# Optimization experiments

Measured on AMD Instinct MI355X. Metric: run time of the kernel, lower is better.

Reference implementation:

```python
import jax, jax.numpy as jnp
import numpy as np

N_EMBD = 1024
N_HEADS = 16
HEAD_SIZE = N_EMBD // N_HEADS
B, T = 1, 4096
LN_EPS = 1e-5


def setup_inputs() -> dict:
    key = jax.random.key(0)
    ks = jax.random.split(key, 12)
    s = lambda fan_in: 1.0 / np.sqrt(fan_in)
    return {
        "x": jax.random.normal(ks[0], (B, T, N_EMBD), dtype=jnp.float32),
        # per-head Q/K/V projections (no bias), stacked over heads: [H, C, hd]
        "Wq": jax.random.normal(ks[1], (N_HEADS, N_EMBD, HEAD_SIZE), dtype=jnp.float32) * s(N_EMBD),
        "Wk": jax.random.normal(ks[2], (N_HEADS, N_EMBD, HEAD_SIZE), dtype=jnp.float32) * s(N_EMBD),
        "Wv": jax.random.normal(ks[3], (N_HEADS, N_EMBD, HEAD_SIZE), dtype=jnp.float32) * s(N_EMBD),
        # output projection (with bias)
        "Wp": jax.random.normal(ks[4], (N_EMBD, N_EMBD), dtype=jnp.float32) * s(N_EMBD),
        "bp": jnp.zeros((N_EMBD,), dtype=jnp.float32),
        # FFN: Linear(C, 4C) -> ReLU -> Linear(4C, C)
        "W1": jax.random.normal(ks[5], (N_EMBD, 4 * N_EMBD), dtype=jnp.float32) * s(N_EMBD),
        "b1": jnp.zeros((4 * N_EMBD,), dtype=jnp.float32),
        "W2": jax.random.normal(ks[6], (4 * N_EMBD, N_EMBD), dtype=jnp.float32) * s(4 * N_EMBD),
        "b2": jnp.zeros((N_EMBD,), dtype=jnp.float32),
        # LayerNorms
        "g1": jnp.ones((N_EMBD,), dtype=jnp.float32),
        "be1": jnp.zeros((N_EMBD,), dtype=jnp.float32),
        "g2": jnp.ones((N_EMBD,), dtype=jnp.float32),
        "be2": jnp.zeros((N_EMBD,), dtype=jnp.float32),
    }


def _layernorm(x, gamma, beta):
    mu = jnp.mean(x, axis=-1, keepdims=True)
    var = jnp.mean(jnp.square(x - mu), axis=-1, keepdims=True)
    return (x - mu) * jax.lax.rsqrt(var + LN_EPS) * gamma + beta


def _block(x, Wq, Wk, Wv, Wp, bp, W1, b1, W2, b2, g1, be1, g2, be2):
    Bn, Tn, C = x.shape
    h = _layernorm(x, g1, be1)
    # per-head projections: [B, H, T, hd]
    q = jnp.einsum("btc,hcd->bhtd", h, Wq)
    k = jnp.einsum("btc,hcd->bhtd", h, Wk)
    v = jnp.einsum("btc,hcd->bhtd", h, Wv)
    # NOTE: original scales by C**-0.5 where C = n_embd (not head_size)
    scores = jnp.einsum("bhtd,bhsd->bhts", q, k) * (C ** -0.5)
    causal = jnp.tril(jnp.ones((Tn, Tn), dtype=bool))
    scores = jnp.where(causal, scores, -jnp.inf)
    w = jax.nn.softmax(scores, axis=-1)
    attn = jnp.einsum("bhts,bhsd->bhtd", w, v)
    # concat heads: [B, T, H*hd] = [B, T, C]
    attn = attn.transpose(0, 2, 1, 3).reshape(Bn, Tn, C)
    x = x + attn @ Wp + bp
    h2 = _layernorm(x, g2, be2)
    ff = jax.nn.relu(h2 @ W1 + b1) @ W2 + b2
    return x + ff


def reference(x, Wq, Wk, Wv, Wp, bp, W1, b1, W2, b2, g1, be1, g2, be2):
    return _block(x, Wq, Wk, Wv, Wp, bp, W1, b1, W2, b2, g1, be1, g2, be2)
```

## Files before the change

### kernel.cpp

```cpp
#include <hip/hip_runtime.h>
#include <cstdint>

typedef __attribute__((ext_vector_type(8))) short bf16x8;
typedef __attribute__((ext_vector_type(4))) float f32x4;
typedef __attribute__((ext_vector_type(16))) float f32x16;
typedef __attribute__((ext_vector_type(4))) unsigned int u32x4;

__device__ __forceinline__ short f2b(float f) {
  unsigned u = __builtin_bit_cast(unsigned, f);
  unsigned r = (u + 0x7fffu + ((u >> 16) & 1u)) >> 16;
  return (short)(unsigned short)r;
}
__device__ __forceinline__ float b2f(short s) {
  unsigned u = ((unsigned)(unsigned short)s) << 16;
  return __builtin_bit_cast(float, u);
}

__device__ __forceinline__ void gload16(void* lds_dst, const void* gsrc) {
  __builtin_amdgcn_global_load_lds(
      (const __attribute__((address_space(1))) void*)gsrc,
      (__attribute__((address_space(3))) void*)lds_dst, 16, 0, 0);
}

__device__ __forceinline__ unsigned cvtpk(float a, float b) {
// ... 115 lines not shown
}

__global__ void vtrans(const short* __restrict__ qkv, short* __restrict__ Vt)
{
  __shared__ short tl[32][33];
  const int t0 = blockIdx.x * 32;
  const int c0 = blockIdx.y * 32;
  const int head = c0 >> 6, d0 = c0 & 63;
  const int tx = threadIdx.x;
#pragma unroll
  for (int i2 = 0; i2 < 4; ++i2) {
    int i = threadIdx.y + i2 * 8;
    tl[i][tx] = qkv[(long)(t0 + i) * 3072 + 2048 + c0 + tx];
  }
  __syncthreads();
#pragma unroll
  for (int i2 = 0; i2 < 4; ++i2) {
    int i = threadIdx.y + i2 * 8;
    Vt[(long)head * 262144 + (long)(d0 + i) * 4096 + t0 + tx] = tl[tx][i];
  }
}

__global__ __launch_bounds__(256)
void layernorm_bf16(const float* __restrict__ x, const float* __restrict__ g,
                    const float* __restrict__ be, short* __restrict__ outp)
{
  const int row = blockIdx.x;
  const int t = threadIdx.x;
  const float4 v = ((const float4*)(x + (long)row * 1024))[t];
  float s = v.x + v.y + v.z + v.w;
  float ss = v.x * v.x + v.y * v.y + v.z * v.z + v.w * v.w;
#pragma unroll
  for (int off = 1; off < 64; off <<= 1) {
    s += __shfl_xor(s, off);
    ss += __shfl_xor(ss, off);
  }
  __shared__ float red[8];
  const int wave = t >> 6, lane = t & 63;
  if (lane == 0) { red[wave] = s; red[4 + wave] = ss; }
  __syncthreads();
  s = red[0] + red[1] + red[2] + red[3];
  ss = red[4] + red[5] + red[6] + red[7];
  const float mu = s * (1.f / 1024.f);
  const float rstd = rsqrtf(ss * (1.f / 1024.f) - mu * mu + 1e-5f);
  const float4 gv = ((const float4*)g)[t];
  const float4 bv = ((const float4*)be)[t];
  short4 ov;
  ov.x = f2b((v.x - mu) * rstd * gv.x + bv.x);
  ov.y = f2b((v.y - mu) * rstd * gv.y + bv.y);
  ov.z = f2b((v.z - mu) * rstd * gv.z + bv.z);
  ov.w = f2b((v.w - mu) * rstd * gv.w + bv.w);
  *(short4*)(outp + (long)row * 1024 + t * 4) = ov;
}

template<int EPI>
__global__ __launch_bounds__(512, 2)
void gemm128(const short* __restrict__ A, const short* __restrict__ Bt,
             int N, int K, int NT,
             short* __restrict__ Cb, float* __restrict__ Cf,
             const float* __restrict__ bias, const float* __restrict__ resid)
{
  __shared__ __align__(16) short As[2 * 8192];
  __shared__ __align__(16) short Bs[2 * 8192];
  const int tid = threadIdx.x;
  const int lane = tid & 63;
  const int wave = tid >> 6;
  const int wm = wave >> 2;
  const int wn = wave & 3;
  const int l15 = lane & 15, lg = lane >> 4;

  const int nwg = gridDim.x * gridDim.y;
  const int lin = blockIdx.y * gridDim.x + blockIdx.x;
  const int swz = (lin & 7) * (nwg >> 3) + (lin >> 3);
  const long m0 = (long)(swz / gridDim.x) * 128;
  const long n0 = (long)(swz % gridDim.x) * 128;

  const int rloc = lane >> 3;
  const int csrc = (lane & 7) ^ rloc;
  const short* Ag = A + (m0 + wave * 8 + rloc) * K + csrc * 8;
  const short* Bg = Bt + (n0 + wave * 8 + rloc) * K + csrc * 8;
  const int wbase = wave * 512;

  f32x4 acc[4][2] = {};

#define STAGE128(buf, kt)                                                     \
  do {                                                                        \
    gload16(As + (buf) * 8192 + wbase, Ag + (kt));                            \
    gload16(As + (buf) * 8192 + 4096 + wbase, Ag + (long)64 * K + (kt));      \
    gload16(Bs + (buf) * 8192 + wbase, Bg + (kt));                            \
    gload16(Bs + (buf) * 8192 + 4096 + wbase, Bg + (long)64 * K + (kt));      \
  } while (0)

  STAGE128(0, 0);
  STAGE128(1, 64);
  asm volatile("s_waitcnt vmcnt(4)" ::: "memory");
  __builtin_amdgcn_sched_barrier(0);
  __builtin_amdgcn_s_barrier();
  __builtin_amdgcn_sched_barrier(0);

  const int cA = l15 & 7;
  for (int t = 0; t < NT; ++t) {
    const char* Ab = (const char*)(As + (t & 1) * 8192);
    const char* Bb = (const char*)(Bs + (t & 1) * 8192);
#pragma unroll
    for (int kk = 0; kk < 2; ++kk) {
      bf16x8 af[4], bk[2];
#pragma unroll
      for (int mi = 0; mi < 4; ++mi)
        af[mi] = *(const bf16x8*)(Ab + (wm * 64 + mi * 16 + l15) * 128 + 16 * ((kk * 4 + lg) ^ cA));
#pragma unroll
      for (int ni = 0; ni < 2; ++ni)
        bk[ni] = *(const bf16x8*)(Bb + (wn * 32 + ni * 16 + l15) * 128 + 16 * ((kk * 4 + lg) ^ cA));
      __builtin_amdgcn_s_setprio(1);
#pragma unroll
      for (int mi = 0; mi < 4; ++mi)
#pragma unroll
        for (int ni = 0; ni < 2; ++ni)
          acc[mi][ni] = __builtin_amdgcn_mfma_f32_16x16x32_bf16(af[mi], bk[ni], acc[mi][ni], 0, 0, 0);
      __builtin_amdgcn_s_setprio(0);
    }
    if (t == NT - 1) break;
    __builtin_amdgcn_s_barrier();
    __builtin_amdgcn_sched_barrier(0);
    if (t + 2 < NT) {
      STAGE128(t & 1, (long)(t + 2) * 64);
      asm volatile("s_waitcnt vmcnt(4)" ::: "memory");
    } else {
      asm volatile("s_waitcnt vmcnt(0)" ::: "memory");
    }
    __builtin_amdgcn_sched_barrier(0);
    __builtin_amdgcn_s_barrier();
    __builtin_amdgcn_sched_barrier(0);
  }
#undef STAGE128

#pragma unroll
  for (int mi = 0; mi < 4; ++mi) {
#pragma unroll
    for (int ni = 0; ni < 2; ++ni) {
      const long col = n0 + wn * 32 + ni * 16 + l15;
#pragma unroll
      for (int r = 0; r < 4; ++r) {
        const long row = m0 + wm * 64 + mi * 16 + lg * 4 + r;
        const long idx = row * N + col;
        float v = acc[mi][ni][r];
        if (EPI == 0) {
          Cb[idx] = f2b(v);
        } else {
          Cf[idx] = v + bias[col] + resid[idx];
        }
      }
    }
  }
}

__device__ __forceinline__ void stage256(short* AsB, short* BsB,
                                         const short* Ag, const short* Bg,
                                         long kt, int K, int ldsoff)
{
#pragma unroll
  for (int p = 0; p < 4; ++p)
    gload16(AsB + p * 4096 + ldsoff, Ag + (long)p * 64 * K + kt);
#pragma unroll
  for (int p = 0; p < 4; ++p)
    gload16(BsB + p * 4096 + ldsoff, Bg + (long)p * 64 * K + kt);
}

template<int EPI>
__global__ __launch_bounds__(512, 2)
void gemm256(const short* __restrict__ A, const short* __restrict__ Bt,
             int N, int K, int NT,
             short* __restrict__ Cb, const float* __restrict__ bias)
{
  __shared__ __align__(16) short As[2 * 16384];
  __shared__ __align__(16) short Bs[2 * 16384];
  const int tid = threadIdx.x;
  const int lane = tid & 63;
  const int wave = tid >> 6;
  const int wm = wave >> 2;
  const int wn = wave & 3;
  const int l15 = lane & 15, lg = lane >> 4;

  const int nwg = gridDim.x * gridDim.y;
  const int lin = blockIdx.y * gridDim.x + blockIdx.x;
  const int swz = (lin & 7) * (nwg >> 3) + (lin >> 3);
  const long m0 = (long)(swz / gridDim.x) * 256;
  const long n0 = (long)(swz % gridDim.x) * 256;

  const int trow = tid >> 3;
  const int csrc = (tid & 7) ^ (trow & 7);
  const short* Ag = A + (m0 + trow) * K + csrc * 8;
  const short* Bg = Bt + (n0 + trow) * K + csrc * 8;
  const int ldsoff = wave * 512;

  f32x4 acc[8][4] = {};

  stage256(As, Bs, Ag, Bg, 0, K, ldsoff);
  asm volatile("s_waitcnt vmcnt(0)" ::: "memory");
  __builtin_amdgcn_sched_barrier(0);
  __builtin_amdgcn_s_barrier();
  __builtin_amdgcn_sched_barrier(0);

  const int cA = l15 & 7;
  for (int t = 0; t < NT; ++t) {
    const char* Ab = (const char*)(As + (t & 1) * 16384);
    const char* Bb = (const char*)(Bs + (t & 1) * 16384);
    short* Asn = As + ((t + 1) & 1) * 16384;
    short* Bsn = Bs + ((t + 1) & 1) * 16384;
    const bool more = (t + 1 < NT);
    const long ktn = (long)(t + 1) * 64;
    bf16x8 bk[4];
#pragma unroll
    for (int ph = 0; ph < 4; ++ph) {
      const int kk = ph >> 1;
      const int mh = (ph & 1) * 4;
      bf16x8 af[4];
#pragma unroll
      for (int mi = 0; mi < 4; ++mi)
        af[mi] = *(const bf16x8*)(Ab + (wm * 128 + (mh + mi) * 16 + l15) * 128 + 16 * ((kk * 4 + lg) ^ cA));
      if ((ph & 1) == 0) {
#pragma unroll
        for (int ni = 0; ni < 4; ++ni)
          bk[ni] = *(const bf16x8*)(Bb + (wn * 64 + ni * 16 + l15) * 128 + 16 * ((kk * 4 + lg) ^ cA));
      }
      if (more && ph == 0) {
#pragma unroll
        for (int p = 0; p < 4; ++p)
          gload16(Asn + p * 4096 + ldsoff, Ag + (long)p * 64 * K + ktn);
      }
      if (more && ph == 1) {
#pragma unroll
        for (int p = 0; p < 4; ++p)
          gload16(Bsn + p * 4096 + ldsoff, Bg + (long)p * 64 * K + ktn);
      }
      __builtin_amdgcn_s_barrier();
      asm volatile("s_waitcnt lgkmcnt(0)" ::: "memory");
      __builtin_amdgcn_sched_barrier(0);
      __builtin_amdgcn_s_setprio(1);
#pragma unroll
      for (int mi = 0; mi < 4; ++mi)
#pragma unroll
        for (int ni = 0; ni < 4; ++ni)
          acc[mh + mi][ni] = __builtin_amdgcn_mfma_f32_16x16x32_bf16(af[mi], bk[ni], acc[mh + mi][ni], 0, 0, 0);
      __builtin_amdgcn_s_setprio(0);
      if (ph == 3 && more) {
        asm volatile("s_waitcnt vmcnt(0)" ::: "memory");
        __builtin_amdgcn_sched_barrier(0);
      }
      __builtin_amdgcn_s_barrier();
      __builtin_amdgcn_sched_barrier(0);
    }
  }

#pragma unroll
  for (int mi = 0; mi < 8; ++mi) {
#pragma unroll
    for (int ni = 0; ni < 4; ++ni) {
      const long col = n0 + wn * 64 + ni * 16 + l15;
      const float bb = (EPI == 2) ? bias[col] : 0.f;
#pragma unroll
      for (int r = 0; r < 4; ++r) {
        const long row = m0 + wm * 128 + mi * 16 + lg * 4 + r;
        float v = acc[mi][ni][r];
        if (EPI == 2) { v += bb; v = v > 0.f ? v : 0.f; }
        Cb[row * N + col] = f2b(v);
      }
    }
  }
}

__device__ __forceinline__ void stage_k32(short* lds, const short* gRowBase)
{
  const int lane = threadIdx.x & 63;
  const int rloc = lane >> 3;
  const int cs = (lane & 7) ^ rloc;
#pragma unroll
  for (int p = 0; p < 4; ++p)
    gload16(lds + p * 512, gRowBase + (long)(p * 8 + rloc) * 3072 + cs * 8);
}
__device__ __forceinline__ void stage_v32(short* lds, const short* vHeadBase, int t0)
{
  const int lane = threadIdx.x & 63;
  const int rloc = lane >> 3;
  const int cs = (lane & 7) ^ rloc;
#pragma unroll
  for (int p = 0; p < 4; ++p) {
    const int row = p * 8 + rloc;
    const int d = row + ((cs & 4) << 3);
    gload16(lds + p * 512, vHeadBase + (long)d * 4096 + t0 + (cs & 3) * 8);
  }
}

__global__ __launch_bounds__(256)
void attn_fwd6(const short* __restrict__ qkv, const short* __restrict__ Vt,
               short* __restrict__ outp)
{
  __shared__ __align__(16) short POOL[4 * 4096];
  __shared__ float lAll[64];
  short* const OB = POOL;

  const int tid = threadIdx.x;
  const int lane = tid & 63;
  const int wave = tid >> 6;
  const int wq = wave & 1;
  const int ks = wave >> 1;
  const int l31 = lane & 31;
  const int h = lane >> 5;
  const int rs = l31 & 7;

  const int id = blockIdx.x;
  const int head = ((id & 7) << 1) | (id >> 8);
  const int bx = (id >> 3) & 31;

  const short* Qg = qkv + head * 64;
  const short* Kg = qkv + 1024 + head * 64;
  const short* Vg = Vt + (long)head * 262144;

  short* Kw = POOL + wave * 4096;

  bf16x8 onesf;
#pragma unroll
  for (int j = 0; j < 8; ++j) onesf[j] = (short)0x3F80;

  for (int ph = 0; ph < 2; ++ph) {
    const int qsuper = ph ? (63 - bx) : bx;
    const int q0 = qsuper * 64 + wq * 32;
    const int q = q0 + l31;
    const int nt = qsuper + 1;

    bf16x8 qf[4];
#pragma unroll
    for (int d = 0; d < 4; ++d) {
      bf16x8 tq = *(const bf16x8*)(Qg + (long)q * 3072 + d * 16 + h * 8);
#pragma unroll
      for (int j = 0; j < 8; ++j) tq[j] = f2b(b2f(tq[j]) * (0.03125f * 1.44269504f));
      qf[d] = tq;
    }

    f32x16 o0 = {}, o1 = {}, lacc = {};

    stage_k32(Kw, Kg + (long)(ks * 32) * 3072);
    stage_v32(Kw + 2048, Vg, ks * 32);

    for (int t = 0; t < nt; ++t) {
      asm volatile("s_waitcnt vmcnt(0)" ::: "memory");
      __builtin_amdgcn_sched_barrier(0);
      const char* Kb = (const char*)Kw;
      const char* Vb = Kb + 4096;
      const bf16x8 kf0 = *(const bf16x8*)(Kb + l31 * 128 + 16 * ((0 + h) ^ rs));
      const bf16x8 kf1 = *(const bf16x8*)(Kb + l31 * 128 + 16 * ((2 + h) ^ rs));
      const bf16x8 kf2 = *(const bf16x8*)(Kb + l31 * 128 + 16 * ((4 + h) ^ rs));
      const bf16x8 kf3 = *(const bf16x8*)(Kb + l31 * 128 + 16 * ((6 + h) ^ rs));
      const bf16x8 vf00 = *(const bf16x8*)(Vb + l31 * 128 + 16 * ((0 + h) ^ rs));
      const bf16x8 vf01 = *(const bf16x8*)(Vb + l31 * 128 + 16 * ((2 + h) ^ rs));
      const bf16x8 vf10 = *(const bf16x8*)(Vb + l31 * 128 + 16 * ((4 + h) ^ rs));
      const bf16x8 vf11 = *(const bf16x8*)(Vb + l31 * 128 + 16 * ((6 + h) ^ rs));
      asm volatile("s_waitcnt lgkmcnt(0)" ::: "memory");
      __builtin_amdgcn_sched_barrier(0);
      if (t + 1 < nt) {
        stage_k32(Kw, Kg + (long)((t + 1) * 64 + ks * 32) * 3072);
        stage_v32(Kw + 2048, Vg, (t + 1) * 64 + ks * 32);
      }
      f32x16 s = {};
      __builtin_amdgcn_s_setprio(1);
      s = __builtin_amdgcn_mfma_f32_32x32x16_bf16(kf0, qf[0], s, 0, 0, 0);
      s = __builtin_amdgcn_mfma_f32_32x32x16_bf16(kf1, qf[1], s, 0, 0, 0);
      s = __builtin_amdgcn_mfma_f32_32x32x16_bf16(kf2, qf[2], s, 0, 0, 0);
      s = __builtin_amdgcn_mfma_f32_32x32x16_bf16(kf3, qf[3], s, 0, 0, 0);
      __builtin_amdgcn_s_setprio(0);
      if (t == qsuper) {
        const int kb0 = t * 64 + ks * 32 + 4 * h;
#pragma unroll
        for (int r = 0; r < 16; ++r) {
          const int k0 = kb0 + (r & 3) + 8 * (r >> 2);
          if (k0 > q) s[r] = -INFINITY;
        }
      }
#pragma unroll
      for (int r = 0; r < 16; ++r) s[r] = exp2x(s[r]);
      unsigned P0 = cvtpk(s[0], s[1]),   P1 = cvtpk(s[2], s[3]);
      unsigned P2 = cvtpk(s[4], s[5]),   P3 = cvtpk(s[6], s[7]);
      unsigned P4 = cvtpk(s[8], s[9]),   P5 = cvtpk(s[10], s[11]);
      unsigned P6 = cvtpk(s[12], s[13]), P7 = cvtpk(s[14], s[15]);
      plswap(P0, P2); plswap(P1, P3); plswap(P4, P6); plswap(P5, P7);
      u32x4 f0, f1;
      f0[0] = P0; f0[1] = P1; f0[2] = P2; f0[3] = P3;
      f1[0] = P4; f1[1] = P5; f1[2] = P6; f1[3] = P7;
      const bf16x8 pa0 = __builtin_bit_cast(bf16x8, f0);
      const bf16x8 pa1 = __builtin_bit_cast(bf16x8, f1);
      __builtin_amdgcn_s_setprio(1);
      o0 = __builtin_amdgcn_mfma_f32_32x32x16_bf16(pa0, vf00, o0, 0, 0, 0);
      o0 = __builtin_amdgcn_mfma_f32_32x32x16_bf16(pa1, vf01, o0, 0, 0, 0);
      o1 = __builtin_amdgcn_mfma_f32_32x32x16_bf16(pa0, vf10, o1, 0, 0, 0);
      o1 = __builtin_amdgcn_mfma_f32_32x32x16_bf16(pa1, vf11, o1, 0, 0, 0);
      lacc = __builtin_amdgcn_mfma_f32_32x32x16_bf16(pa0, onesf, lacc, 0, 0, 0);
      lacc = __builtin_amdgcn_mfma_f32_32x32x16_bf16(pa1, onesf, lacc, 0, 0, 0);
      __builtin_amdgcn_s_setprio(0);
    }

    __syncthreads();
    if (ks == 1) {
#pragma unroll
      for (int r = 0; r < 16; ++r) {
        const int qq = wq * 32 + (r & 3) + 8 * (r >> 2) + 4 * h;
        OB[qq * 64 + l31] = f2b(o0[r]);
        OB[qq * 64 + 32 + l31] = f2b(o1[r]);
      }
      if (l31 == 0) {
#pragma unroll
        for (int r = 0; r < 16; ++r) {
          const int qq = wq * 32 + (r & 3) + 8 * (r >> 2) + 4 * h;
          lAll[qq] = lacc[r];
        }
      }
    }
    __syncthreads();
    if (ks == 0) {
#pragma unroll
      for (int r = 0; r < 16; ++r) {
        const int qq = wq * 32 + (r & 3) + 8 * (r >> 2) + 4 * h;
        const float inv = 1.f / (lacc[r] + lAll[qq]);
        const long qr = (long)qsuper * 64 + qq;
        const float v0 = o0[r] + b2f(OB[qq * 64 + l31]);
        const float v1 = o1[r] + b2f(OB[qq * 64 + 32 + l31]);
        outp[qr * 1024 + head * 64 + l31] = f2b(v0 * inv);
        outp[qr * 1024 + head * 64 + 32 + l31] = f2b(v1 * inv);
      }
    }
    __syncthreads();
  }
}

extern "C" void kernel_launch(void* const* d_in, const int* in_sizes, int n_in,
                              void* d_out, int out_size, void* d_ws, size_t ws_size,
                              hipStream_t stream)
{
  (void)in_sizes; (void)n_in; (void)out_size; (void)ws_size;
  const float* x   = (const float*)d_in[0];
  const float* Wq  = (const float*)d_in[1];
  const float* Wk  = (const float*)d_in[2];
  const float* Wv  = (const float*)d_in[3];
  const float* Wp  = (const float*)d_in[4];
  const float* bp  = (const float*)d_in[5];
  const float* W1  = (const float*)d_in[6];
  const float* b1  = (const float*)d_in[7];
  const float* W2  = (const float*)d_in[8];
  const float* b2  = (const float*)d_in[9];
  const float* g1  = (const float*)d_in[10];
  const float* be1 = (const float*)d_in[11];
  const float* g2  = (const float*)d_in[12];
  const float* be2 = (const float*)d_in[13];
  float* out = (float*)d_out;

  char* ws = (char*)d_ws;
  const size_t MB = 1ull << 20;
  short* WqkvT = (short*)(ws + 0 * MB);
  short* WpT   = (short*)(ws + 6 * MB);
  short* W1T   = (short*)(ws + 8 * MB);
  short* W2T   = (short*)(ws + 16 * MB);
  short* hbuf  = (short*)(ws + 24 * MB);
  short* qkvb  = (short*)(ws + 32 * MB);
  short* attnb = (short*)(ws + 56 * MB);
  float* x1    = (float*)(ws + 64 * MB);
  short* Vtb   = (short*)(ws + 64 * MB);

  prep_all<<<16384, 256, 0, stream>>>(Wq, Wk, Wv, Wp, W1, W2, x, g1, be1,
                                      WqkvT, WpT, W1T, W2T, hbuf);
  gemm256<0><<<dim3(12, 16), 512, 0, stream>>>(hbuf, WqkvT, 3072, 1024, 16,
                                               qkvb, nullptr);
  vtrans<<<dim3(128, 32), dim3(32, 8), 0, stream>>>(qkvb, Vtb);
  attn_fwd6<<<512, 256, 0, stream>>>(qkvb, Vtb, attnb);
  gemm128<1><<<dim3(8, 32), 512, 0, stream>>>(attnb, WpT, 1024, 1024, 16,
                                              nullptr, x1, bp, x);
  layernorm_bf16<<<4096, 256, 0, stream>>>(x1, g2, be2, hbuf);
  gemm256<2><<<dim3(16, 16), 512, 0, stream>>>(hbuf, W1T, 4096, 1024, 16,
                                               qkvb, b1);
  gemm128<1><<<dim3(8, 32), 512, 0, stream>>>(qkvb, W2T, 1024, 4096, 64,
                                              nullptr, out, b2, x1);
}
```

Measured before the change: 246.8 us.

## Split attention KV range by tile parity and merge partials in a separate kernel

```diff
diff --git a/kernel.cpp b/kernel.cpp
--- a/kernel.cpp
+++ b/kernel.cpp
@@ -431,8 +431,9 @@
 }
 
 __global__ __launch_bounds__(256)
-void attn_fwd6(const short* __restrict__ qkv, const short* __restrict__ Vt,
-               short* __restrict__ outp)
+void attn_fwd7(const short* __restrict__ qkv, const short* __restrict__ Vt,
+               short* __restrict__ P0buf, short* __restrict__ P1buf,
+               float* __restrict__ lbuf)
 {
   __shared__ __align__(16) short POOL[4 * 4096];
   __shared__ float lAll[64];
@@ -448,12 +449,17 @@
   const int rs = l31 & 7;
 
   const int id = blockIdx.x;
-  const int head = ((id & 7) << 1) | (id >> 8);
-  const int bx = (id >> 3) & 31;
+  const int xcd = id & 7;
+  const int k = id >> 3;
+  const int head = (xcd << 1) | (k & 1);
+  const int qp = k >> 1;
+  const int qsuper = 63 - (qp >> 1);
+  const int parity = qp & 1;
 
   const short* Qg = qkv + head * 64;
   const short* Kg = qkv + 1024 + head * 64;
   const short* Vg = Vt + (long)head * 262144;
+  short* Pout = parity ? P1buf : P0buf;
 
   short* Kw = POOL + wave * 4096;
 
@@ -461,113 +467,133 @@
 #pragma unroll
   for (int j = 0; j < 8; ++j) onesf[j] = (short)0x3F80;
 
-  for (int ph = 0; ph < 2; ++ph) {
-    const int qsuper = ph ? (63 - bx) : bx;
-    const int q0 = qsuper * 64 + wq * 32;
-    const int q = q0 + l31;
-    const int nt = qsuper + 1;
-
-    bf16x8 qf[4];
-#pragma unroll
-    for (int d = 0; d < 4; ++d) {
-      bf16x8 tq = *(const bf16x8*)(Qg + (long)q * 3072 + d * 16 + h * 8);
-#pragma unroll
-      for (int j = 0; j < 8; ++j) tq[j] = f2b(b2f(tq[j]) * (0.03125f * 1.44269504f));
-      qf[d] = tq;
-    }
-
-    f32x16 o0 = {}, o1 = {}, lacc = {};
-
-    stage_k32(Kw, Kg + (long)(ks * 32) * 3072);
-    stage_v32(Kw + 2048, Vg, ks * 32);
-
-    for (int t = 0; t < nt; ++t) {
-      asm volatile("s_waitcnt vmcnt(0)" ::: "memory");
-      __builtin_amdgcn_sched_barrier(0);
-      const char* Kb = (const char*)Kw;
-      const char* Vb = Kb + 4096;
-      const bf16x8 kf0 = *(const bf16x8*)(Kb + l31 * 128 + 16 * ((0 + h) ^ rs));
-      const bf16x8 kf1 = *(const bf16x8*)(Kb + l31 * 128 + 16 * ((2 + h) ^ rs));
-      const bf16x8 kf2 = *(const bf16x8*)(Kb + l31 * 128 + 16 * ((4 + h) ^ rs));
-      const bf16x8 kf3 = *(const bf16x8*)(Kb + l31 * 128 + 16 * ((6 + h) ^ rs));
-      const bf16x8 vf00 = *(const bf16x8*)(Vb + l31 * 128 + 16 * ((0 + h) ^ rs));
-      const bf16x8 vf01 = *(const bf16x8*)(Vb + l31 * 128 + 16 * ((2 + h) ^ rs));
-      const bf16x8 vf10 = *(const bf16x8*)(Vb + l31 * 128 + 16 * ((4 + h) ^ rs));
-      const bf16x8 vf11 = *(const bf16x8*)(Vb + l31 * 128 + 16 * ((6 + h) ^ rs));
-      asm volatile("s_waitcnt lgkmcnt(0)" ::: "memory");
-      __builtin_amdgcn_sched_barrier(0);
-      if (t + 1 < nt) {
-        stage_k32(Kw, Kg + (long)((t + 1) * 64 + ks * 32) * 3072);
-        stage_v32(Kw + 2048, Vg, (t + 1) * 64 + ks * 32);
-      }
-      f32x16 s = {};
-      __builtin_amdgcn_s_setprio(1);
-      s = __builtin_amdgcn_mfma_f32_32x32x16_bf16(kf0, qf[0], s, 0, 0, 0);
-      s = __builtin_amdgcn_mfma_f32_32x32x16_bf16(kf1, qf[1], s, 0, 0, 0);
-      s = __builtin_amdgcn_mfma_f32_32x32x16_bf16(kf2, qf[2], s, 0, 0, 0);
-      s = __builtin_amdgcn_mfma_f32_32x32x16_bf16(kf3, qf[3], s, 0, 0, 0);
-      __builtin_amdgcn_s_setprio(0);
-      if (t == qsuper) {
-        const int kb0 = t * 64 + ks * 32 + 4 * h;
-#pragma unroll
-        for (int r = 0; r < 16; ++r) {
-          const int k0 = kb0 + (r & 3) + 8 * (r >> 2);
-          if (k0 > q) s[r] = -INFINITY;
-        }
-      }
-#pragma unroll
-      for (int r = 0; r < 16; ++r) s[r] = exp2x(s[r]);
-      unsigned P0 = cvtpk(s[0], s[1]),   P1 = cvtpk(s[2], s[3]);
-      unsigned P2 = cvtpk(s[4], s[5]),   P3 = cvtpk(s[6], s[7]);
-      unsigned P4 = cvtpk(s[8], s[9]),   P5 = cvtpk(s[10], s[11]);
-      unsigned P6 = cvtpk(s[12], s[13]), P7 = cvtpk(s[14], s[15]);
-      plswap(P0, P2); plswap(P1, P3); plswap(P4, P6); plswap(P5, P7);
-      u32x4 f0, f1;
-      f0[0] = P0; f0[1] = P1; f0[2] = P2; f0[3] = P3;
-      f1[0] = P4; f1[1] = P5; f1[2] = P6; f1[3] = P7;
-      const bf16x8 pa0 = __builtin_bit_cast(bf16x8, f0);
-      const bf16x8 pa1 = __builtin_bit_cast(bf16x8, f1);
-      __builtin_amdgcn_s_setprio(1);
-      o0 = __builtin_amdgcn_mfma_f32_32x32x16_bf16(pa0, vf00, o0, 0, 0, 0);
-      o0 = __builtin_amdgcn_mfma_f32_32x32x16_bf16(pa1, vf01, o0, 0, 0, 0);
-      o1 = __builtin_amdgcn_mfma_f32_32x32x16_bf16(pa0, vf10, o1, 0, 0, 0);
-      o1 = __builtin_amdgcn_mfma_f32_32x32x16_bf16(pa1, vf11, o1, 0, 0, 0);
-      lacc = __builtin_amdgcn_mfma_f32_32x32x16_bf16(pa0, onesf, lacc, 0, 0, 0);
-      lacc = __builtin_amdgcn_mfma_f32_32x32x16_bf16(pa1, onesf, lacc, 0, 0, 0);
-      __builtin_amdgcn_s_setprio(0);
-    }
-
-    __syncthreads();
-    if (ks == 1) {
+  const int q0 = qsuper * 64 + wq * 32;
+  const int q = q0 + l31;
+  const int nt = qsuper + 1;
+
+  bf16x8 qf[4];
+#pragma unroll
+  for (int d = 0; d < 4; ++d) {
+    bf16x8 tq = *(const bf16x8*)(Qg + (long)q * 3072 + d * 16 + h * 8);
+#pragma unroll
+    for (int j = 0; j < 8; ++j) tq[j] = f2b(b2f(tq[j]) * (0.03125f * 1.44269504f));
+    qf[d] = tq;
+  }
+
+  f32x16 o0 = {}, o1 = {}, lacc = {};
+
+  if (parity < nt) {
+    stage_k32(Kw, Kg + (long)(parity * 64 + ks * 32) * 3072);
+    stage_v32(Kw + 2048, Vg, parity * 64 + ks * 32);
+  }
+
+  for (int t = parity; t < nt; t += 2) {
+    asm volatile("s_waitcnt vmcnt(0)" ::: "memory");
+    __builtin_amdgcn_sched_barrier(0);
+    const char* Kb = (const char*)Kw;
+    const char* Vb = Kb + 4096;
+    const bf16x8 kf0 = *(const bf16x8*)(Kb + l31 * 128 + 16 * ((0 + h) ^ rs));
+    const bf16x8 kf1 = *(const bf16x8*)(Kb + l31 * 128 + 16 * ((2 + h) ^ rs));
+    const bf16x8 kf2 = *(const bf16x8*)(Kb + l31 * 128 + 16 * ((4 + h) ^ rs));
+    const bf16x8 kf3 = *(const bf16x8*)(Kb + l31 * 128 + 16 * ((6 + h) ^ rs));
+    const bf16x8 vf00 = *(const bf16x8*)(Vb + l31 * 128 + 16 * ((0 + h) ^ rs));
+    const bf16x8 vf01 = *(const bf16x8*)(Vb + l31 * 128 + 16 * ((2 + h) ^ rs));
+    const bf16x8 vf10 = *(const bf16x8*)(Vb + l31 * 128 + 16 * ((4 + h) ^ rs));
+    const bf16x8 vf11 = *(const bf16x8*)(Vb + l31 * 128 + 16 * ((6 + h) ^ rs));
+    asm volatile("s_waitcnt lgkmcnt(0)" ::: "memory");
+    __builtin_amdgcn_sched_barrier(0);
+    if (t + 2 < nt) {
+      stage_k32(Kw, Kg + (long)((t + 2) * 64 + ks * 32) * 3072);
+      stage_v32(Kw + 2048, Vg, (t + 2) * 64 + ks * 32);
+    }
+    f32x16 s = {};
+    __builtin_amdgcn_s_setprio(1);
+    s = __builtin_amdgcn_mfma_f32_32x32x16_bf16(kf0, qf[0], s, 0, 0, 0);
+    s = __builtin_amdgcn_mfma_f32_32x32x16_bf16(kf1, qf[1], s, 0, 0, 0);
+    s = __builtin_amdgcn_mfma_f32_32x32x16_bf16(kf2, qf[2], s, 0, 0, 0);
+    s = __builtin_amdgcn_mfma_f32_32x32x16_bf16(kf3, qf[3], s, 0, 0, 0);
+    __builtin_amdgcn_s_setprio(0);
+    if (t == qsuper) {
+      const int kb0 = t * 64 + ks * 32 + 4 * h;
+#pragma unroll
+      for (int r = 0; r < 16; ++r) {
+        const int k0 = kb0 + (r & 3) + 8 * (r >> 2);
+        if (k0 > q) s[r] = -INFINITY;
+      }
+    }
+#pragma unroll
+    for (int r = 0; r < 16; ++r) s[r] = exp2x(s[r]);
+    unsigned P0 = cvtpk(s[0], s[1]),   P1 = cvtpk(s[2], s[3]);
+    unsigned P2 = cvtpk(s[4], s[5]),   P3 = cvtpk(s[6], s[7]);
+    unsigned P4 = cvtpk(s[8], s[9]),   P5 = cvtpk(s[10], s[11]);
+    unsigned P6 = cvtpk(s[12], s[13]), P7 = cvtpk(s[14], s[15]);
+    plswap(P0, P2); plswap(P1, P3); plswap(P4, P6); plswap(P5, P7);
+    u32x4 f0, f1;
+    f0[0] = P0; f0[1] = P1; f0[2] = P2; f0[3] = P3;
+    f1[0] = P4; f1[1] = P5; f1[2] = P6; f1[3] = P7;
+    const bf16x8 pa0 = __builtin_bit_cast(bf16x8, f0);
+    const bf16x8 pa1 = __builtin_bit_cast(bf16x8, f1);
+    __builtin_amdgcn_s_setprio(1);
+    o0 = __builtin_amdgcn_mfma_f32_32x32x16_bf16(pa0, vf00, o0, 0, 0, 0);
+    o0 = __builtin_amdgcn_mfma_f32_32x32x16_bf16(pa1, vf01, o0, 0, 0, 0);
+    o1 = __builtin_amdgcn_mfma_f32_32x32x16_bf16(pa0, vf10, o1, 0, 0, 0);
+    o1 = __builtin_amdgcn_mfma_f32_32x32x16_bf16(pa1, vf11, o1, 0, 0, 0);
+    lacc = __builtin_amdgcn_mfma_f32_32x32x16_bf16(pa0, onesf, lacc, 0, 0, 0);
+    lacc = __builtin_amdgcn_mfma_f32_32x32x16_bf16(pa1, onesf, lacc, 0, 0, 0);
+    __builtin_amdgcn_s_setprio(0);
+  }
+
+  __syncthreads();
+  if (ks == 1) {
+#pragma unroll
+    for (int r = 0; r < 16; ++r) {
+      const int qq = wq * 32 + (r & 3) + 8 * (r >> 2) + 4 * h;
+      OB[qq * 64 + l31] = f2b(o0[r]);
+      OB[qq * 64 + 32 + l31] = f2b(o1[r]);
+    }
+    if (l31 == 0) {
 #pragma unroll
       for (int r = 0; r < 16; ++r) {
         const int qq = wq * 32 + (r & 3) + 8 * (r >> 2) + 4 * h;
-        OB[qq * 64 + l31] = f2b(o0[r]);
-        OB[qq * 64 + 32 + l31] = f2b(o1[r]);
-      }
-      if (l31 == 0) {
-#pragma unroll
-        for (int r = 0; r < 16; ++r) {
-          const int qq = wq * 32 + (r & 3) + 8 * (r >> 2) + 4 * h;
-          lAll[qq] = lacc[r];
-        }
-      }
-    }
-    __syncthreads();
-    if (ks == 0) {
-#pragma unroll
-      for (int r = 0; r < 16; ++r) {
-        const int qq = wq * 32 + (r & 3) + 8 * (r >> 2) + 4 * h;
-        const float inv = 1.f / (lacc[r] + lAll[qq]);
-        const long qr = (long)qsuper * 64 + qq;
-        const float v0 = o0[r] + b2f(OB[qq * 64 + l31]);
-        const float v1 = o1[r] + b2f(OB[qq * 64 + 32 + l31]);
-        outp[qr * 1024 + head * 64 + l31] = f2b(v0 * inv);
-        outp[qr * 1024 + head * 64 + 32 + l31] = f2b(v1 * inv);
-      }
-    }
-    __syncthreads();
-  }
+        lAll[qq] = lacc[r];
+      }
+    }
+  }
+  __syncthreads();
+  if (ks == 0) {
+#pragma unroll
+    for (int r = 0; r < 16; ++r) {
+      const int qq = wq * 32 + (r & 3) + 8 * (r >> 2) + 4 * h;
+      const long qr = (long)qsuper * 64 + qq;
+      const float v0 = o0[r] + b2f(OB[qq * 64 + l31]);
+      const float v1 = o1[r] + b2f(OB[qq * 64 + 32 + l31]);
+      Pout[qr * 1024 + head * 64 + l31] = f2b(v0);
+      Pout[qr * 1024 + head * 64 + 32 + l31] = f2b(v1);
+      if (l31 == 0)
+        lbuf[(long)parity * 65536 + head * 4096 + qr] = lacc[r] + lAll[qq];
+    }
+  }
+}
+
+__global__ __launch_bounds__(256)
+void merge_attn(const short* __restrict__ P0, const short* __restrict__ P1,
+                const float* __restrict__ lbuf, short* __restrict__ outp)
+{
+  const int q = blockIdx.x;
+  const int t = threadIdx.x;
+  const int head = t >> 4;
+  const float l0 = lbuf[head * 4096 + q];
+  const float l1 = lbuf[65536 + head * 4096 + q];
+  const float inv = 1.f / (l0 + l1);
+  const long base = (long)q * 1024 + t * 4;
+  short4 a = *(const short4*)(P0 + base);
+  short4 b = *(const short4*)(P1 + base);
+  short4 o;
+  o.x = f2b((b2f(a.x) + b2f(b.x)) * inv);
+  o.y = f2b((b2f(a.y) + b2f(b.y)) * inv);
+  o.z = f2b((b2f(a.z) + b2f(b.z)) * inv);
+  o.w = f2b((b2f(a.w) + b2f(b.w)) * inv);
+  *(short4*)(outp + base) = o;
 }
 
 extern "C" void kernel_launch(void* const* d_in, const int* in_sizes, int n_in,
@@ -602,13 +628,16 @@
   short* attnb = (short*)(ws + 56 * MB);
   float* x1    = (float*)(ws + 64 * MB);
   short* Vtb   = (short*)(ws + 64 * MB);
+  float* lbuf  = (float*)(ws + 0 * MB);
+  short* P1buf = hbuf;
 
   prep_all<<<16384, 256, 0, stream>>>(Wq, Wk, Wv, Wp, W1, W2, x, g1, be1,
                                       WqkvT, WpT, W1T, W2T, hbuf);
   gemm256<0><<<dim3(12, 16), 512, 0, stream>>>(hbuf, WqkvT, 3072, 1024, 16,
                                                qkvb, nullptr);
   vtrans<<<dim3(128, 32), dim3(32, 8), 0, stream>>>(qkvb, Vtb);
-  attn_fwd6<<<512, 256, 0, stream>>>(qkvb, Vtb, attnb);
+  attn_fwd7<<<2048, 256, 0, stream>>>(qkvb, Vtb, attnb, P1buf, lbuf);
+  merge_attn<<<4096, 256, 0, stream>>>(attnb, P1buf, lbuf, attnb);
   gemm128<1><<<dim3(8, 32), 512, 0, stream>>>(attnb, WpT, 1024, 1024, 16,
                                               nullptr, x1, bp, x);
   layernorm_bf16<<<4096, 256, 0, stream>>>(x1, g2, be2, hbuf);
```

Result: slower. 254.8 us (+3.2%).

## Process both paired query tiles in one K/V sweep in attention

Applied to the files above, without the earlier changes.

```diff
diff --git a/kernel.cpp b/kernel.cpp
--- a/kernel.cpp
+++ b/kernel.cpp
@@ -431,7 +431,7 @@
 }
 
 __global__ __launch_bounds__(256)
-void attn_fwd6(const short* __restrict__ qkv, const short* __restrict__ Vt,
+void attn_fwd8(const short* __restrict__ qkv, const short* __restrict__ Vt,
                short* __restrict__ outp)
 {
   __shared__ __align__(16) short POOL[4 * 4096];
@@ -450,6 +450,7 @@
   const int id = blockIdx.x;
   const int head = ((id & 7) << 1) | (id >> 8);
   const int bx = (id >> 3) & 31;
+  const int qsA = bx, qsB = 63 - bx;
 
   const short* Qg = qkv + head * 64;
   const short* Kg = qkv + 1024 + head * 64;
@@ -461,66 +462,78 @@
 #pragma unroll
   for (int j = 0; j < 8; ++j) onesf[j] = (short)0x3F80;
 
-  for (int ph = 0; ph < 2; ++ph) {
-    const int qsuper = ph ? (63 - bx) : bx;
-    const int q0 = qsuper * 64 + wq * 32;
-    const int q = q0 + l31;
-    const int nt = qsuper + 1;
-
-    bf16x8 qf[4];
-#pragma unroll
-    for (int d = 0; d < 4; ++d) {
-      bf16x8 tq = *(const bf16x8*)(Qg + (long)q * 3072 + d * 16 + h * 8);
-#pragma unroll
-      for (int j = 0; j < 8; ++j) tq[j] = f2b(b2f(tq[j]) * (0.03125f * 1.44269504f));
-      qf[d] = tq;
-    }
-
-    f32x16 o0 = {}, o1 = {}, lacc = {};
-
-    stage_k32(Kw, Kg + (long)(ks * 32) * 3072);
-    stage_v32(Kw + 2048, Vg, ks * 32);
-
-    for (int t = 0; t < nt; ++t) {
-      asm volatile("s_waitcnt vmcnt(0)" ::: "memory");
-      __builtin_amdgcn_sched_barrier(0);
-      const char* Kb = (const char*)Kw;
-      const char* Vb = Kb + 4096;
-      const bf16x8 kf0 = *(const bf16x8*)(Kb + l31 * 128 + 16 * ((0 + h) ^ rs));
-      const bf16x8 kf1 = *(const bf16x8*)(Kb + l31 * 128 + 16 * ((2 + h) ^ rs));
-      const bf16x8 kf2 = *(const bf16x8*)(Kb + l31 * 128 + 16 * ((4 + h) ^ rs));
-      const bf16x8 kf3 = *(const bf16x8*)(Kb + l31 * 128 + 16 * ((6 + h) ^ rs));
-      const bf16x8 vf00 = *(const bf16x8*)(Vb + l31 * 128 + 16 * ((0 + h) ^ rs));
-      const bf16x8 vf01 = *(const bf16x8*)(Vb + l31 * 128 + 16 * ((2 + h) ^ rs));
-      const bf16x8 vf10 = *(const bf16x8*)(Vb + l31 * 128 + 16 * ((4 + h) ^ rs));
-      const bf16x8 vf11 = *(const bf16x8*)(Vb + l31 * 128 + 16 * ((6 + h) ^ rs));
-      asm volatile("s_waitcnt lgkmcnt(0)" ::: "memory");
-      __builtin_amdgcn_sched_barrier(0);
-      if (t + 1 < nt) {
-        stage_k32(Kw, Kg + (long)((t + 1) * 64 + ks * 32) * 3072);
-        stage_v32(Kw + 2048, Vg, (t + 1) * 64 + ks * 32);
-      }
-      f32x16 s = {};
-      __builtin_amdgcn_s_setprio(1);
-      s = __builtin_amdgcn_mfma_f32_32x32x16_bf16(kf0, qf[0], s, 0, 0, 0);
-      s = __builtin_amdgcn_mfma_f32_32x32x16_bf16(kf1, qf[1], s, 0, 0, 0);
-      s = __builtin_amdgcn_mfma_f32_32x32x16_bf16(kf2, qf[2], s, 0, 0, 0);
-      s = __builtin_amdgcn_mfma_f32_32x32x16_bf16(kf3, qf[3], s, 0, 0, 0);
-      __builtin_amdgcn_s_setprio(0);
-      if (t == qsuper) {
-        const int kb0 = t * 64 + ks * 32 + 4 * h;
-#pragma unroll
-        for (int r = 0; r < 16; ++r) {
-          const int k0 = kb0 + (r & 3) + 8 * (r >> 2);
-          if (k0 > q) s[r] = -INFINITY;
-        }
-      }
-#pragma unroll
-      for (int r = 0; r < 16; ++r) s[r] = exp2x(s[r]);
-      unsigned P0 = cvtpk(s[0], s[1]),   P1 = cvtpk(s[2], s[3]);
-      unsigned P2 = cvtpk(s[4], s[5]),   P3 = cvtpk(s[6], s[7]);
-      unsigned P4 = cvtpk(s[8], s[9]),   P5 = cvtpk(s[10], s[11]);
-      unsigned P6 = cvtpk(s[12], s[13]), P7 = cvtpk(s[14], s[15]);
+  const int q0A = qsA * 64 + wq * 32, qA = q0A + l31;
+  const int q0B = qsB * 64 + wq * 32, qB = q0B + l31;
+  const int nt = qsB + 1;
+
+  bf16x8 qfA[4], qfB[4];
+#pragma unroll
+  for (int d = 0; d < 4; ++d) {
+    bf16x8 ta = *(const bf16x8*)(Qg + (long)qA * 3072 + d * 16 + h * 8);
+    bf16x8 tb = *(const bf16x8*)(Qg + (long)qB * 3072 + d * 16 + h * 8);
+#pragma unroll
+    for (int j = 0; j < 8; ++j) {
+      ta[j] = f2b(b2f(ta[j]) * (0.03125f * 1.44269504f));
+      tb[j] = f2b(b2f(tb[j]) * (0.03125f * 1.44269504f));
+    }
+    qfA[d] = ta;
+    qfB[d] = tb;
+  }
+
+  f32x16 oA0 = {}, oA1 = {}, lA = {};
+  f32x16 oB0 = {}, oB1 = {}, lB = {};
+
+  stage_k32(Kw, Kg + (long)(ks * 32) * 3072);
+  stage_v32(Kw + 2048, Vg, ks * 32);
+
+  for (int t = 0; t < nt; ++t) {
+    asm volatile("s_waitcnt vmcnt(0)" ::: "memory");
+    __builtin_amdgcn_sched_barrier(0);
+    const char* Kb = (const char*)Kw;
+    const char* Vb = Kb + 4096;
+    const bf16x8 kf0 = *(const bf16x8*)(Kb + l31 * 128 + 16 * ((0 + h) ^ rs));
+    const bf16x8 kf1 = *(const bf16x8*)(Kb + l31 * 128 + 16 * ((2 + h) ^ rs));
+    const bf16x8 kf2 = *(const bf16x8*)(Kb + l31 * 128 + 16 * ((4 + h) ^ rs));
+    const bf16x8 kf3 = *(const bf16x8*)(Kb + l31 * 128 + 16 * ((6 + h) ^ rs));
+    const bf16x8 vf00 = *(const bf16x8*)(Vb + l31 * 128 + 16 * ((0 + h) ^ rs));
+    const bf16x8 vf01 = *(const bf16x8*)(Vb + l31 * 128 + 16 * ((2 + h) ^ rs));
+    const bf16x8 vf10 = *(const bf16x8*)(Vb + l31 * 128 + 16 * ((4 + h) ^ rs));
+    const bf16x8 vf11 = *(const bf16x8*)(Vb + l31 * 128 + 16 * ((6 + h) ^ rs));
+    asm volatile("s_waitcnt lgkmcnt(0)" ::: "memory");
+    __builtin_amdgcn_sched_barrier(0);
+    if (t + 1 < nt) {
+      stage_k32(Kw, Kg + (long)((t + 1) * 64 + ks * 32) * 3072);
+      stage_v32(Kw + 2048, Vg, (t + 1) * 64 + ks * 32);
+    }
+    const bool doA = (t <= qsA);
+    f32x16 sB = {}, sA = {};
+    __builtin_amdgcn_s_setprio(1);
+    sB = __builtin_amdgcn_mfma_f32_32x32x16_bf16(kf0, qfB[0], sB, 0, 0, 0);
+    sB = __builtin_amdgcn_mfma_f32_32x32x16_bf16(kf1, qfB[1], sB, 0, 0, 0);
+    sB = __builtin_amdgcn_mfma_f32_32x32x16_bf16(kf2, qfB[2], sB, 0, 0, 0);
+    sB = __builtin_amdgcn_mfma_f32_32x32x16_bf16(kf3, qfB[3], sB, 0, 0, 0);
+    if (doA) {
+      sA = __builtin_amdgcn_mfma_f32_32x32x16_bf16(kf0, qfA[0], sA, 0, 0, 0);
+      sA = __builtin_amdgcn_mfma_f32_32x32x16_bf16(kf1, qfA[1], sA, 0, 0, 0);
+      sA = __builtin_amdgcn_mfma_f32_32x32x16_bf16(kf2, qfA[2], sA, 0, 0, 0);
+      sA = __builtin_amdgcn_mfma_f32_32x32x16_bf16(kf3, qfA[3], sA, 0, 0, 0);
+    }
+    __builtin_amdgcn_s_setprio(0);
+    if (t == qsB) {
+      const int kb0 = t * 64 + ks * 32 + 4 * h;
+#pragma unroll
+      for (int r = 0; r < 16; ++r) {
+        const int k0 = kb0 + (r & 3) + 8 * (r >> 2);
+        if (k0 > qB) sB[r] = -INFINITY;
+      }
+    }
+#pragma unroll
+    for (int r = 0; r < 16; ++r) sB[r] = exp2x(sB[r]);
+    {
+      unsigned P0 = cvtpk(sB[0], sB[1]),   P1 = cvtpk(sB[2], sB[3]);
+      unsigned P2 = cvtpk(sB[4], sB[5]),   P3 = cvtpk(sB[6], sB[7]);
+      unsigned P4 = cvtpk(sB[8], sB[9]),   P5 = cvtpk(sB[10], sB[11]);
+      unsigned P6 = cvtpk(sB[12], sB[13]), P7 = cvtpk(sB[14], sB[15]);
       plswap(P0, P2); plswap(P1, P3); plswap(P4, P6); plswap(P5, P7);
       u32x4 f0, f1;
       f0[0] = P0; f0[1] = P1; f0[2] = P2; f0[3] = P3;
@@ -528,45 +541,103 @@
       const bf16x8 pa0 = __builtin_bit_cast(bf16x8, f0);
       const bf16x8 pa1 = __builtin_bit_cast(bf16x8, f1);
       __builtin_amdgcn_s_setprio(1);
-      o0 = __builtin_amdgcn_mfma_f32_32x32x16_bf16(pa0, vf00, o0, 0, 0, 0);
-      o0 = __builtin_amdgcn_mfma_f32_32x32x16_bf16(pa1, vf01, o0, 0, 0, 0);
-      o1 = __builtin_amdgcn_mfma_f32_32x32x16_bf16(pa0, vf10, o1, 0, 0, 0);
-      o1 = __builtin_amdgcn_mfma_f32_32x32x16_bf16(pa1, vf11, o1, 0, 0, 0);
-      lacc = __builtin_amdgcn_mfma_f32_32x32x16_bf16(pa0, onesf, lacc, 0, 0, 0);
-      lacc = __builtin_amdgcn_mfma_f32_32x32x16_bf16(pa1, onesf, lacc, 0, 0, 0);
+      oB0 = __builtin_amdgcn_mfma_f32_32x32x16_bf16(pa0, vf00, oB0, 0, 0, 0);
+      oB0 = __builtin_amdgcn_mfma_f32_32x32x16_bf16(pa1, vf01, oB0, 0, 0, 0);
+      oB1 = __builtin_amdgcn_mfma_f32_32x32x16_bf16(pa0, vf10, oB1, 0, 0, 0);
+      oB1 = __builtin_amdgcn_mfma_f32_32x32x16_bf16(pa1, vf11, oB1, 0, 0, 0);
+      lB = __builtin_amdgcn_mfma_f32_32x32x16_bf16(pa0, onesf, lB, 0, 0, 0);
+      lB = __builtin_amdgcn_mfma_f32_32x32x16_bf16(pa1, onesf, lB, 0, 0, 0);
       __builtin_amdgcn_s_setprio(0);
     }
-
-    __syncthreads();
-    if (ks == 1) {
+    if (doA) {
+      if (t == qsA) {
+        const int kb0 = t * 64 + ks * 32 + 4 * h;
+#pragma unroll
+        for (int r = 0; r < 16; ++r) {
+          const int k0 = kb0 + (r & 3) + 8 * (r >> 2);
+          if (k0 > qA) sA[r] = -INFINITY;
+        }
+      }
+#pragma unroll
+      for (int r = 0; r < 16; ++r) sA[r] = exp2x(sA[r]);
+      unsigned P0 = cvtpk(sA[0], sA[1]),   P1 = cvtpk(sA[2], sA[3]);
+      unsigned P2 = cvtpk(sA[4], sA[5]),   P3 = cvtpk(sA[6], sA[7]);
+      unsigned P4 = cvtpk(sA[8], sA[9]),   P5 = cvtpk(sA[10], sA[11]);
+      unsigned P6 = cvtpk(sA[12], sA[13]), P7 = cvtpk(sA[14], sA[15]);
+      plswap(P0, P2); plswap(P1, P3); plswap(P4, P6); plswap(P5, P7);
+      u32x4 f0, f1;
+      f0[0] = P0; f0[1] = P1; f0[2] = P2; f0[3] = P3;
+      f1[0] = P4; f1[1] = P5; f1[2] = P6; f1[3] = P7;
+      const bf16x8 pa0 = __builtin_bit_cast(bf16x8, f0);
+      const bf16x8 pa1 = __builtin_bit_cast(bf16x8, f1);
+      __builtin_amdgcn_s_setprio(1);
+      oA0 = __builtin_amdgcn_mfma_f32_32x32x16_bf16(pa0, vf00, oA0, 0, 0, 0);
+      oA0 = __builtin_amdgcn_mfma_f32_32x32x16_bf16(pa1, vf01, oA0, 0, 0, 0);
+      oA1 = __builtin_amdgcn_mfma_f32_32x32x16_bf16(pa0, vf10, oA1, 0, 0, 0);
+      oA1 = __builtin_amdgcn_mfma_f32_32x32x16_bf16(pa1, vf11, oA1, 0, 0, 0);
+      lA = __builtin_amdgcn_mfma_f32_32x32x16_bf16(pa0, onesf, lA, 0, 0, 0);
+      lA = __builtin_amdgcn_mfma_f32_32x32x16_bf16(pa1, onesf, lA, 0, 0, 0);
+      __builtin_amdgcn_s_setprio(0);
+    }
+  }
+
+  __syncthreads();
+  if (ks == 1) {
+#pragma unroll
+    for (int r = 0; r < 16; ++r) {
+      const int qq = wq * 32 + (r & 3) + 8 * (r >> 2) + 4 * h;
+      OB[qq * 64 + l31] = f2b(oB0[r]);
+      OB[qq * 64 + 32 + l31] = f2b(oB1[r]);
+    }
+    if (l31 == 0) {
 #pragma unroll
       for (int r = 0; r < 16; ++r) {
         const int qq = wq * 32 + (r & 3) + 8 * (r >> 2) + 4 * h;
-        OB[qq * 64 + l31] = f2b(o0[r]);
-        OB[qq * 64 + 32 + l31] = f2b(o1[r]);
-      }
-      if (l31 == 0) {
-#pragma unroll
-        for (int r = 0; r < 16; ++r) {
-          const int qq = wq * 32 + (r & 3) + 8 * (r >> 2) + 4 * h;
-          lAll[qq] = lacc[r];
-        }
-      }
-    }
-    __syncthreads();
-    if (ks == 0) {
+        lAll[qq] = lB[r];
+      }
+    }
+  }
+  __syncthreads();
+  if (ks == 0) {
+#pragma unroll
+    for (int r = 0; r < 16; ++r) {
+      const int qq = wq * 32 + (r & 3) + 8 * (r >> 2) + 4 * h;
+      const float inv = 1.f / (lB[r] + lAll[qq]);
+      const long qr = (long)qsB * 64 + qq;
+      const float v0 = oB0[r] + b2f(OB[qq * 64 + l31]);
+      const float v1 = oB1[r] + b2f(OB[qq * 64 + 32 + l31]);
+      outp[qr * 1024 + head * 64 + l31] = f2b(v0 * inv);
+      outp[qr * 1024 + head * 64 + 32 + l31] = f2b(v1 * inv);
+    }
+  }
+  __syncthreads();
+  if (ks == 1) {
+#pragma unroll
+    for (int r = 0; r < 16; ++r) {
+      const int qq = wq * 32 + (r & 3) + 8 * (r >> 2) + 4 * h;
+      OB[qq * 64 + l31] = f2b(oA0[r]);
+      OB[qq * 64 + 32 + l31] = f2b(oA1[r]);
+    }
+    if (l31 == 0) {
 #pragma unroll
       for (int r = 0; r < 16; ++r) {
         const int qq = wq * 32 + (r & 3) + 8 * (r >> 2) + 4 * h;
-        const float inv = 1.f / (lacc[r] + lAll[qq]);
-        const long qr = (long)qsuper * 64 + qq;
-        const float v0 = o0[r] + b2f(OB[qq * 64 + l31]);
-        const float v1 = o1[r] + b2f(OB[qq * 64 + 32 + l31]);
-        outp[qr * 1024 + head * 64 + l31] = f2b(v0 * inv);
-        outp[qr * 1024 + head * 64 + 32 + l31] = f2b(v1 * inv);
-      }
-    }
-    __syncthreads();
+        lAll[qq] = lA[r];
+      }
+    }
+  }
+  __syncthreads();
+  if (ks == 0) {
+#pragma unroll
+    for (int r = 0; r < 16; ++r) {
+      const int qq = wq * 32 + (r & 3) + 8 * (r >> 2) + 4 * h;
+      const float inv = 1.f / (lA[r] + lAll[qq]);
+      const long qr = (long)qsA * 64 + qq;
+      const float v0 = oA0[r] + b2f(OB[qq * 64 + l31]);
+      const float v1 = oA1[r] + b2f(OB[qq * 64 + 32 + l31]);
+      outp[qr * 1024 + head * 64 + l31] = f2b(v0 * inv);
+      outp[qr * 1024 + head * 64 + 32 + l31] = f2b(v1 * inv);
+    }
   }
 }
 
@@ -608,7 +679,7 @@
   gemm256<0><<<dim3(12, 16), 512, 0, stream>>>(hbuf, WqkvT, 3072, 1024, 16,
                                                qkvb, nullptr);
   vtrans<<<dim3(128, 32), dim3(32, 8), 0, stream>>>(qkvb, Vtb);
-  attn_fwd6<<<512, 256, 0, stream>>>(qkvb, Vtb, attnb);
+  attn_fwd8<<<512, 256, 0, stream>>>(qkvb, Vtb, attnb);
   gemm128<1><<<dim3(8, 32), 512, 0, stream>>>(attnb, WpT, 1024, 1024, 16,
                                               nullptr, x1, bp, x);
   layernorm_bf16<<<4096, 256, 0, stream>>>(x1, g2, be2, hbuf);
```

Measured after the change: 249.3 us. No clear change (+1.0%).

## Split-K the FFN down-projection GEMM into two halves with a separate reduction kernel

Applied to the files above, without the earlier changes.

```diff
diff --git a/kernel.cpp b/kernel.cpp
--- a/kernel.cpp
+++ b/kernel.cpp
@@ -291,6 +291,123 @@
       }
     }
   }
+}
+
+__global__ __launch_bounds__(512, 2)
+void gemm128sk(const short* __restrict__ A, const short* __restrict__ Bt,
+               int N, int K, int NT,
+               short* __restrict__ p0, short* __restrict__ p1)
+{
+  __shared__ __align__(16) short As[2 * 8192];
+  __shared__ __align__(16) short Bs[2 * 8192];
+  const int tid = threadIdx.x;
+  const int lane = tid & 63;
+  const int wave = tid >> 6;
+  const int wm = wave >> 2;
+  const int wn = wave & 3;
+  const int l15 = lane & 15, lg = lane >> 4;
+
+  const int nwg = gridDim.x * gridDim.y;
+  const int lin = blockIdx.y * gridDim.x + blockIdx.x;
+  const int swz = (lin & 7) * (nwg >> 3) + (lin >> 3);
+  const int my = swz >> 3;
+  const int half = my >> 5;
+  const long m0 = (long)(my & 31) * 128;
+  const long n0 = (long)(swz & 7) * 128;
+  const long k0 = (long)half * 2048;
+  short* const Cb = half ? p1 : p0;
+
+  const int rloc = lane >> 3;
+  const int csrc = (lane & 7) ^ rloc;
+  const short* Ag = A + (m0 + wave * 8 + rloc) * K + csrc * 8 + k0;
+  const short* Bg = Bt + (n0 + wave * 8 + rloc) * K + csrc * 8 + k0;
+  const int wbase = wave * 512;
+
+  f32x4 acc[4][2] = {};
+
+#define STAGESK(buf, kt)                                                      \
+  do {                                                                        \
+    gload16(As + (buf) * 8192 + wbase, Ag + (kt));                            \
+    gload16(As + (buf) * 8192 + 4096 + wbase, Ag + (long)64 * K + (kt));      \
+    gload16(Bs + (buf) * 8192 + wbase, Bg + (kt));                            \
+    gload16(Bs + (buf) * 8192 + 4096 + wbase, Bg + (long)64 * K + (kt));      \
+  } while (0)
+
+  STAGESK(0, 0);
+  STAGESK(1, 64);
+  asm volatile("s_waitcnt vmcnt(4)" ::: "memory");
+  __builtin_amdgcn_sched_barrier(0);
+  __builtin_amdgcn_s_barrier();
+  __builtin_amdgcn_sched_barrier(0);
+
+  const int cA = l15 & 7;
+  for (int t = 0; t < NT; ++t) {
+    const char* Ab = (const char*)(As + (t & 1) * 8192);
+    const char* Bb = (const char*)(Bs + (t & 1) * 8192);
+#pragma unroll
+    for (int kk = 0; kk < 2; ++kk) {
+      bf16x8 af[4], bk[2];
+#pragma unroll
+      for (int mi = 0; mi < 4; ++mi)
+        af[mi] = *(const bf16x8*)(Ab + (wm * 64 + mi * 16 + l15) * 128 + 16 * ((kk * 4 + lg) ^ cA));
+#pragma unroll
+      for (int ni = 0; ni < 2; ++ni)
+        bk[ni] = *(const bf16x8*)(Bb + (wn * 32 + ni * 16 + l15) * 128 + 16 * ((kk * 4 + lg) ^ cA));
+      __builtin_amdgcn_s_setprio(1);
+#pragma unroll
+      for (int mi = 0; mi < 4; ++mi)
+#pragma unroll
+        for (int ni = 0; ni < 2; ++ni)
+          acc[mi][ni] = __builtin_amdgcn_mfma_f32_16x16x32_bf16(af[mi], bk[ni], acc[mi][ni], 0, 0, 0);
+      __builtin_amdgcn_s_setprio(0);
+    }
+    if (t == NT - 1) break;
+    __builtin_amdgcn_s_barrier();
+    __builtin_amdgcn_sched_barrier(0);
+    if (t + 2 < NT) {
+      STAGESK(t & 1, (long)(t + 2) * 64);
+      asm volatile("s_waitcnt vmcnt(4)" ::: "memory");
+    } else {
+      asm volatile("s_waitcnt vmcnt(0)" ::: "memory");
+    }
+    __builtin_amdgcn_sched_barrier(0);
+    __builtin_amdgcn_s_barrier();
+    __builtin_amdgcn_sched_barrier(0);
+  }
+#undef STAGESK
+
+#pragma unroll
+  for (int mi = 0; mi < 4; ++mi) {
+#pragma unroll
+    for (int ni = 0; ni < 2; ++ni) {
+      const long col = n0 + wn * 32 + ni * 16 + l15;
+#pragma unroll
+      for (int r = 0; r < 4; ++r) {
+        const long row = m0 + wm * 64 + mi * 16 + lg * 4 + r;
+        Cb[row * N + col] = f2b(acc[mi][ni][r]);
+      }
+    }
+  }
+}
+
+__global__ __launch_bounds__(256)
+void reduce_ffn2(const short* __restrict__ p0, const short* __restrict__ p1,
+                 const float* __restrict__ bias, const float* __restrict__ resid,
+                 float* __restrict__ outp)
+{
+  const long row = blockIdx.x;
+  const int t = threadIdx.x;
+  const long base = row * 1024 + t * 4;
+  const short4 a = *(const short4*)(p0 + base);
+  const short4 b = *(const short4*)(p1 + base);
+  const float4 rv = *(const float4*)(resid + base);
+  const float4 bv = ((const float4*)bias)[t];
+  float4 o;
+  o.x = b2f(a.x) + b2f(b.x) + bv.x + rv.x;
+  o.y = b2f(a.y) + b2f(b.y) + bv.y + rv.y;
+  o.z = b2f(a.z) + b2f(b.z) + bv.z + rv.z;
+  o.w = b2f(a.w) + b2f(b.w) + bv.w + rv.w;
+  *(float4*)(outp + base) = o;
 }
 
 __device__ __forceinline__ void stage256(short* AsB, short* BsB,
@@ -602,6 +719,8 @@
   short* attnb = (short*)(ws + 56 * MB);
   float* x1    = (float*)(ws + 64 * MB);
   short* Vtb   = (short*)(ws + 64 * MB);
+  short* p0buf = (short*)(ws + 0 * MB);
+  short* p1buf = (short*)(ws + 8 * MB);
 
   prep_all<<<16384, 256, 0, stream>>>(Wq, Wk, Wv, Wp, W1, W2, x, g1, be1,
                                       WqkvT, WpT, W1T, W2T, hbuf);
@@ -614,6 +733,7 @@
   layernorm_bf16<<<4096, 256, 0, stream>>>(x1, g2, be2, hbuf);
   gemm256<2><<<dim3(16, 16), 512, 0, stream>>>(hbuf, W1T, 4096, 1024, 16,
                                                qkvb, b1);
-  gemm128<1><<<dim3(8, 32), 512, 0, stream>>>(qkvb, W2T, 1024, 4096, 64,
-                                              nullptr, out, b2, x1);
-}
+  gemm128sk<<<dim3(8, 64), 512, 0, stream>>>(qkvb, W2T, 1024, 4096, 32,
+                                             p0buf, p1buf);
+  reduce_ffn2<<<4096, 256, 0, stream>>>(p0buf, p1buf, b2, x1, out);
+}
```

New measurement: 231.5 us. 6.2% less time.
